# Kernel optimization log

Measured on AMD Instinct MI355X. Metric: run time of the kernel, lower is better.

## Reference

```python
import jax, jax.numpy as jnp
import numpy as np

B = 32768
INPUT_DIM = 2048
D = 2
HIDDEN = 128
V = 20          # output_dim (number of heads)
P = 6           # n_corr_params
R = 10          # r_lora = min(V // 2, 10)


def setup_inputs() -> dict:
    key = jax.random.key(0)
    ks = jax.random.split(key, 12)

    def lin(k, fan_in, shape):
        bound = 1.0 / np.sqrt(fan_in)
        return jax.random.uniform(k, shape, jnp.float32, -bound, bound)

    x = jax.random.normal(ks[0], (B, INPUT_DIM), jnp.float32)
    # encoder: Linear(input_dim, hidden) -> ReLU -> (Dropout=id) -> Linear(hidden, d)
    We1 = lin(ks[1], INPUT_DIM, (INPUT_DIM, HIDDEN))
    be1 = lin(ks[2], INPUT_DIM, (HIDDEN,))
    We2 = lin(ks[3], HIDDEN, (HIDDEN, D))
    be2 = lin(ks[4], HIDDEN, (D,))
    # 20 heads, each Linear(d, hidden) -> ReLU -> Linear(hidden, 6) -> Tanh,
    # stacked into batched weight tensors.
    W1 = lin(ks[5], D, (V, D, HIDDEN))
    b1 = lin(ks[6], D, (V, HIDDEN))
    W2 = lin(ks[7], HIDDEN, (V, HIDDEN, P))
    b2 = lin(ks[8], HIDDEN, (V, P))
    # LoRA params
    lora_A = jax.random.normal(ks[9], (D, R), jnp.float32) * 0.01
    lora_B = jax.random.normal(ks[10], (R, V * P), jnp.float32) * 0.01
    return {"x": x, "We1": We1, "be1": be1, "We2": We2, "be2": be2,
            "W1": W1, "b1": b1, "W2": W2, "b2": b2,
            "lora_A": lora_A, "lora_B": lora_B}


def reference(x, We1, be1, We2, be2, W1, b1, W2, b2, lora_A, lora_B):
    # encoder (nonlinear reduction; dropout is identity in eval)
    z = jax.nn.relu(x @ We1 + be1) @ We2 + be2            # [B, D]
    # all 20 heads as batched GEMMs
    h = jax.nn.relu(jnp.einsum('bd,vdh->bvh', z, W1) + b1)  # [B, V, HIDDEN]
    heads = jnp.tanh(jnp.einsum('bvh,vhp->bvp', h, W2) + b2)  # [B, V, P]
    # LoRA contribution, then outer tanh (note: double tanh, faithful to source)
    lora = (z @ lora_A @ lora_B).reshape(-1, V, P)         # [B, V, P]
    out = jnp.tanh(heads + 0.15 * lora)
    return (out, z)
```

## Files before the change

kernel.cpp:

```cpp
#include <hip/hip_runtime.h>
#include <hip/hip_bf16.h>
#include <cstdint>
#include <cstddef>

#define BDIM   32768
#define KDIM   2048
#define NDIM   128
#define VHEADS 20
#define PDIM   6
#define RLORA  10

#define BK      64
#define NCHUNK  (KDIM / BK)
#define OUT_ELEMS   (BDIM * VHEADS * PDIM)
#define WS_W_BYTES  (KDIM * NDIM * 2)

typedef __attribute__((ext_vector_type(8))) __bf16 bf16x8;
typedef __attribute__((ext_vector_type(4))) float f32x4;
typedef __attribute__((ext_vector_type(2))) float f32x2;
typedef __attribute__((ext_vector_type(4))) unsigned int u32x4;

union FragU { bf16x8 b; u32x4 u; };

__device__ __forceinline__ unsigned int cvt_pk_bf16(float lo, float hi) {
  unsigned int r;
  asm("v_cvt_pk_bf16_f32 %0, %1, %2" : "=v"(r) : "v"(lo), "v"(hi));
  return r;
}

__device__ __forceinline__ void gload_lds16(const void* g, void* l) {
  __builtin_amdgcn_global_load_lds(
      (const __attribute__((address_space(1))) void*)(g),
      (__attribute__((address_space(3))) void*)(l), 16, 0, 0);
}

__device__ __forceinline__ float fast_tanh(float x) {
  float ax = fabsf(x);
  float e  = __expf(-2.0f * ax);
  float t  = __fdividef(1.0f - e, 1.0f + e);
  return copysignf(t, x);
}

__global__ __launch_bounds__(256)
void k0_pack(const float* __restrict__ We1,
             const float* __restrict__ lA,
             const float* __restrict__ lB,
             unsigned short* __restrict__ wsw,
             float* __restrict__ wsM) {
  if (blockIdx.x == 128) {
    int t = threadIdx.x;
    if (t < 2 * VHEADS * PDIM) {
      int d  = t / (VHEADS * PDIM);
      int vp = t - d * (VHEADS * PDIM);
      float s = 0.f;
#pragma unroll
      for (int r = 0; r < RLORA; ++r)
        s = fmaf(lA[d * RLORA + r], lB[r * (VHEADS * PDIM) + vp], s);
      wsM[t] = s;
    }
    return;
  }
  int t    = blockIdx.x * 256 + threadIdx.x;
  int lane = t & 63;
  int blk  = t >> 6;
  int ks   = blk & 1;
  int nt   = (blk >> 1) & 7;
  int c    = blk >> 4;
  int n    = nt * 16 + (lane & 15);
  int kb   = c * 64 + ks * 32 + (lane >> 4) * 8;

  unsigned int u[4];
#pragma unroll
  for (int q = 0; q < 4; ++q) {
    float f0 = We1[(size_t)(kb + 2 * q + 0) * NDIM + n];
    float f1 = We1[(size_t)(kb + 2 * q + 1) * NDIM + n];
    __hip_bfloat16 h0 = __float2bfloat16(f0);
    __hip_bfloat16 h1 = __float2bfloat16(f1);
    u[q] = (unsigned int)*reinterpret_cast<unsigned short*>(&h0) |
           ((unsigned int)*reinterpret_cast<unsigned short*>(&h1) << 16);
  }
  *reinterpret_cast<u32x4*>(wsw + (size_t)t * 8) = u32x4{u[0], u[1], u[2], u[3]};
}

__global__ __launch_bounds__(512, 4)
void k1_fused(const float* __restrict__ x,
              const unsigned short* __restrict__ wp,
              const float* __restrict__ be1,
              const float* __restrict__ We2,
              const float* __restrict__ be2,
              const float* __restrict__ W1,
              const float* __restrict__ b1,
              const float* __restrict__ W2,
              const float* __restrict__ b2,
              const float* __restrict__ M,
              float* __restrict__ out,
              float* __restrict__ zout) {
  __shared__ char ldsA[2][16384] __attribute__((aligned(16)));
  __shared__ char ldsB[2][16384] __attribute__((aligned(16)));
  __shared__ float zpart2[64][2][2];
  __shared__ float zsh[64][2];

  const int tid  = threadIdx.x;
  const int lane = tid & 63;
  const int wv   = tid >> 6;
  const int wr   = wv & 3;
  const int wc   = wv >> 2;
  const int l15  = lane & 15;
  const int kgrp = lane >> 4;
  const int blk  = blockIdx.x;

  f32x4 acc[4];
#pragma unroll
  for (int i = 0; i < 4; ++i) acc[i] = f32x4{0.f, 0.f, 0.f, 0.f};

  auto STAGE = [&](int b, int c) {
#pragma unroll
    for (int q = 0; q < 2; ++q) {
      int s = tid + q * 512;
      int row = s >> 4;
      int g = (s & 15) ^ (row & 7);
      const float* asrc = x + (size_t)(blk * 64 + row) * KDIM + c * BK + g * 4;
      gload_lds16(asrc, &ldsA[b][s * 16]);
    }
#pragma unroll
    for (int q = 0; q < 2; ++q) {
      gload_lds16((const char*)wp + (size_t)c * 16384 + q * 8192 + tid * 16,
                  &ldsB[b][q * 8192 + tid * 16]);
    }
  };

  auto COMPUTE = [&](int b) {
    const int row = wr * 16 + l15;
    const char* abase = &ldsA[b][row * 256];
    const int rx = (row & 7) << 4;
    f32x4 A0 = *(const f32x4*)(abase + (((kgrp * 2 + 0) << 4) ^ rx));
    f32x4 A1 = *(const f32x4*)(abase + (((kgrp * 2 + 1) << 4) ^ rx));
    f32x4 A2 = *(const f32x4*)(abase + 128 + (((kgrp * 2 + 0) << 4) ^ rx));
    f32x4 A3 = *(const f32x4*)(abase + 128 + (((kgrp * 2 + 1) << 4) ^ rx));
    FragU a0, a1;
    a0.u = u32x4{cvt_pk_bf16(A0.x, A0.y), cvt_pk_bf16(A0.z, A0.w),
                 cvt_pk_bf16(A1.x, A1.y), cvt_pk_bf16(A1.z, A1.w)};
    a1.u = u32x4{cvt_pk_bf16(A2.x, A2.y), cvt_pk_bf16(A2.z, A2.w),
                 cvt_pk_bf16(A3.x, A3.y), cvt_pk_bf16(A3.z, A3.w)};
    const char* bbase = &ldsB[b][lane * 16];
#pragma unroll
    for (int nt = 0; nt < 4; ++nt) {
      FragU b0, b1;
      b0.u = *(const u32x4*)(bbase + ((wc * 4 + nt) * 2 + 0) * 1024);
      b1.u = *(const u32x4*)(bbase + ((wc * 4 + nt) * 2 + 1) * 1024);
      acc[nt] = __builtin_amdgcn_mfma_f32_16x16x32_bf16(a0.b, b0.b, acc[nt], 0, 0, 0);
      acc[nt] = __builtin_amdgcn_mfma_f32_16x16x32_bf16(a1.b, b1.b, acc[nt], 0, 0, 0);
    }
  };

  STAGE(0, 0);
  __syncthreads();

#pragma unroll 1
  for (int c = 0; c < NCHUNK; ++c) {
    int b = c & 1;
    if (c + 1 < NCHUNK) STAGE(b ^ 1, c + 1);
    COMPUTE(b);
    __syncthreads();
  }

  float part[4][2];
#pragma unroll
  for (int j = 0; j < 4; ++j) { part[j][0] = 0.f; part[j][1] = 0.f; }
#pragma unroll
  for (int nt = 0; nt < 4; ++nt) {
    int col = (wc * 4 + nt) * 16 + l15;
    float bb = be1[col];
    float w0 = We2[col * 2 + 0];
    float w1 = We2[col * 2 + 1];
#pragma unroll
    for (int j = 0; j < 4; ++j) {
      float h = acc[nt][j] + bb;
      h = h > 0.f ? h : 0.f;
      part[j][0] = fmaf(h, w0, part[j][0]);
      part[j][1] = fmaf(h, w1, part[j][1]);
    }
  }
#pragma unroll
  for (int m = 1; m < 16; m <<= 1) {
#pragma unroll
    for (int j = 0; j < 4; ++j) {
      part[j][0] += __shfl_xor(part[j][0], m, 64);
      part[j][1] += __shfl_xor(part[j][1], m, 64);
    }
  }
  if (l15 == 0) {
#pragma unroll
    for (int j = 0; j < 4; ++j) {
      int rl = wr * 16 + kgrp * 4 + j;
      zpart2[rl][wc][0] = part[j][0];
      zpart2[rl][wc][1] = part[j][1];
    }
  }
  __syncthreads();
  if (tid < 64) {
    float s0 = zpart2[tid][0][0] + zpart2[tid][1][0] + be2[0];
    float s1 = zpart2[tid][0][1] + zpart2[tid][1][1] + be2[1];
    zsh[tid][0] = s0;
    zsh[tid][1] = s1;
    f32x2 zz = {s0, s1};
    *(f32x2*)(zout + (size_t)(blk * 64 + tid) * 2) = zz;
  }
  __syncthreads();

  const int wvu = __builtin_amdgcn_readfirstlane(wv);
  float z0 = zsh[lane][0];
  float z1 = zsh[lane][1];
  float* orow = out + (size_t)(blk * 64 + lane) * (VHEADS * PDIM);

  auto head = [&](int v) {
    const float* w1a = W1 + (size_t)(v * 2 + 0) * NDIM;
    const float* w1b = W1 + (size_t)(v * 2 + 1) * NDIM;
    const float* bb1 = b1 + (size_t)v * NDIM;
    const float* w2  = W2 + (size_t)v * NDIM * PDIM;

    float p[6] = {0.f, 0.f, 0.f, 0.f, 0.f, 0.f};
#pragma unroll 4
    for (int h = 0; h < NDIM; ++h) {
      float hv = fmaf(z0, w1a[h], fmaf(z1, w1b[h], bb1[h]));
      hv = hv > 0.f ? hv : 0.f;
#pragma unroll
      for (int j = 0; j < 6; ++j) p[j] = fmaf(hv, w2[h * 6 + j], p[j]);
    }
    float o[6];
#pragma unroll
    for (int j = 0; j < 6; ++j) {
      float t1 = fast_tanh(p[j] + b2[v * PDIM + j]);
      float lo = fmaf(z0, M[v * PDIM + j], z1 * M[VHEADS * PDIM + v * PDIM + j]);
      o[j] = fast_tanh(fmaf(0.15f, lo, t1));
    }
    float* op = orow + v * PDIM;
    f32x2 o01 = {o[0], o[1]};
    f32x2 o23 = {o[2], o[3]};
    f32x2 o45 = {o[4], o[5]};
    __builtin_nontemporal_store(o01, (f32x2*)(op + 0));
    __builtin_nontemporal_store(o23, (f32x2*)(op + 2));
    __builtin_nontemporal_store(o45, (f32x2*)(op + 4));
  };

  head(wvu);
  head(wvu + 8);
  if (wvu < 4) head(wvu + 16);
}

extern "C" void kernel_launch(void* const* d_in, const int* in_sizes, int n_in,
                              void* d_out, int out_size, void* d_ws, size_t ws_size,
                              hipStream_t stream) {
  const float* x   = (const float*)d_in[0];
  const float* We1 = (const float*)d_in[1];
  const float* be1 = (const float*)d_in[2];
  const float* We2 = (const float*)d_in[3];
  const float* be2 = (const float*)d_in[4];
  const float* W1  = (const float*)d_in[5];
  const float* b1  = (const float*)d_in[6];
  const float* W2  = (const float*)d_in[7];
  const float* b2  = (const float*)d_in[8];
  const float* lA  = (const float*)d_in[9];
  const float* lB  = (const float*)d_in[10];

  float* out  = (float*)d_out;
  float* zout = out + OUT_ELEMS;
  unsigned short* wsw = (unsigned short*)d_ws;
  float* wsM = (float*)((char*)d_ws + WS_W_BYTES);

  hipLaunchKernelGGL(k0_pack, dim3(129), dim3(256), 0, stream,
                     We1, lA, lB, wsw, wsM);
  hipLaunchKernelGGL(k1_fused, dim3(BDIM / 64), dim3(512), 0, stream,
                     x, wsw, be1, We2, be2, W1, b1, W2, b2, wsM, out, zout);
}
```

Before: 102.7 us.

## Keep two K-chunks in flight with explicit vmcnt waits and split barriers

Restructures the main GEMM loop so two chunk loads are outstanding at once, using per-buffer LDS arrays, manual s_waitcnt vmcnt(4) waits and raw s_barrier with sched_barrier fences in place of __syncthreads. The aim is to hide global-to-LDS latency better by letting the next chunk's load overlap compute on the current one, rather than draining all loads each iteration. It relies on hand-counted outstanding loads (4 per stage), so correctness depends on exact instruction counts and on the compiler not inserting extra memory ops. There are now two barriers per chunk instead of one.

```diff
diff --git a/kernel.cpp b/kernel.cpp
--- a/kernel.cpp
+++ b/kernel.cpp
@@ -40,6 +40,8 @@
   float t  = __fdividef(1.0f - e, 1.0f + e);
   return copysignf(t, x);
 }
+
+#define SBAR() __builtin_amdgcn_sched_barrier(0)
 
 __global__ __launch_bounds__(256)
 void k0_pack(const float* __restrict__ We1,
@@ -95,8 +97,10 @@
               const float* __restrict__ M,
               float* __restrict__ out,
               float* __restrict__ zout) {
-  __shared__ char ldsA[2][16384] __attribute__((aligned(16)));
-  __shared__ char ldsB[2][16384] __attribute__((aligned(16)));
+  __shared__ char A0_[16384] __attribute__((aligned(16)));
+  __shared__ char A1_[16384] __attribute__((aligned(16)));
+  __shared__ char B0_[16384] __attribute__((aligned(16)));
+  __shared__ char B1_[16384] __attribute__((aligned(16)));
   __shared__ float zpart2[64][2][2];
   __shared__ float zsh[64][2];
 
@@ -113,25 +117,25 @@
 #pragma unroll
   for (int i = 0; i < 4; ++i) acc[i] = f32x4{0.f, 0.f, 0.f, 0.f};
 
-  auto STAGE = [&](int b, int c) {
+  auto STAGE = [&](char* Ad, char* Bd, int c) {
 #pragma unroll
     for (int q = 0; q < 2; ++q) {
       int s = tid + q * 512;
       int row = s >> 4;
       int g = (s & 15) ^ (row & 7);
       const float* asrc = x + (size_t)(blk * 64 + row) * KDIM + c * BK + g * 4;
-      gload_lds16(asrc, &ldsA[b][s * 16]);
+      gload_lds16(asrc, Ad + s * 16);
     }
 #pragma unroll
     for (int q = 0; q < 2; ++q) {
       gload_lds16((const char*)wp + (size_t)c * 16384 + q * 8192 + tid * 16,
-                  &ldsB[b][q * 8192 + tid * 16]);
+                  Bd + q * 8192 + tid * 16);
     }
   };
 
-  auto COMPUTE = [&](int b) {
+  auto COMPUTE = [&](const char* Ad, const char* Bd) {
     const int row = wr * 16 + l15;
-    const char* abase = &ldsA[b][row * 256];
+    const char* abase = Ad + row * 256;
     const int rx = (row & 7) << 4;
     f32x4 A0 = *(const f32x4*)(abase + (((kgrp * 2 + 0) << 4) ^ rx));
     f32x4 A1 = *(const f32x4*)(abase + (((kgrp * 2 + 1) << 4) ^ rx));
@@ -142,7 +146,7 @@
                  cvt_pk_bf16(A1.x, A1.y), cvt_pk_bf16(A1.z, A1.w)};
     a1.u = u32x4{cvt_pk_bf16(A2.x, A2.y), cvt_pk_bf16(A2.z, A2.w),
                  cvt_pk_bf16(A3.x, A3.y), cvt_pk_bf16(A3.z, A3.w)};
-    const char* bbase = &ldsB[b][lane * 16];
+    const char* bbase = Bd + lane * 16;
 #pragma unroll
     for (int nt = 0; nt < 4; ++nt) {
       FragU b0, b1;
@@ -153,16 +157,34 @@
     }
   };
 
-  STAGE(0, 0);
-  __syncthreads();
+  STAGE(A0_, B0_, 0);
+  STAGE(A1_, B1_, 1);
 
 #pragma unroll 1
-  for (int c = 0; c < NCHUNK; ++c) {
-    int b = c & 1;
-    if (c + 1 < NCHUNK) STAGE(b ^ 1, c + 1);
-    COMPUTE(b);
-    __syncthreads();
-  }
+  for (int cc = 0; cc < NCHUNK / 2 - 1; ++cc) {
+    asm volatile("s_waitcnt vmcnt(4)" ::: "memory");
+    SBAR();
+    __builtin_amdgcn_s_barrier();
+    COMPUTE(A0_, B0_);
+    __builtin_amdgcn_s_barrier();
+    SBAR();
+    STAGE(A0_, B0_, 2 * cc + 2);
+    asm volatile("s_waitcnt vmcnt(4)" ::: "memory");
+    SBAR();
+    __builtin_amdgcn_s_barrier();
+    COMPUTE(A1_, B1_);
+    __builtin_amdgcn_s_barrier();
+    SBAR();
+    STAGE(A1_, B1_, 2 * cc + 3);
+  }
+  asm volatile("s_waitcnt vmcnt(4)" ::: "memory");
+  SBAR();
+  __builtin_amdgcn_s_barrier();
+  COMPUTE(A0_, B0_);
+  asm volatile("s_waitcnt vmcnt(0)" ::: "memory");
+  SBAR();
+  __builtin_amdgcn_s_barrier();
+  COMPUTE(A1_, B1_);
 
   float part[4][2];
 #pragma unroll
```

After: 95.87 us (median of 2 runs). 1.07x faster.

## Halve row tile, load B fragments directly to registers, barrier-free per-wave pipeline

Applied to the files above, without the earlier changes.

The block tile shrinks from 64 to 32 rows with 256 threads and twice as many blocks. Each wave now stages only its own A rows into LDS. The packed We1 fragments are loaded straight into registers with inline global_load_dwordx4 instead of through LDS. The K loop is double-buffered with explicit vmcnt waits and sched barriers in place of __syncthreads, which removes block-wide synchronisation and LDS traffic for B. The cost is that each block re-reads all of We1 from cache, so B-operand global/L2 traffic doubles, and correctness now depends on hand-counted vmcnt values.

```diff
diff --git a/kernel.cpp b/kernel.cpp
--- a/kernel.cpp
+++ b/kernel.cpp
@@ -10,6 +10,7 @@
 #define PDIM   6
 #define RLORA  10
 
+#define BM      32
 #define BK      64
 #define NCHUNK  (KDIM / BK)
 #define OUT_ELEMS   (BDIM * VHEADS * PDIM)
@@ -40,6 +41,11 @@
   float t  = __fdividef(1.0f - e, 1.0f + e);
   return copysignf(t, x);
 }
+
+#define SBAR() __builtin_amdgcn_sched_barrier(0)
+#define GL16(dst, addr, OFFSTR) \
+  asm volatile("global_load_dwordx4 %0, %1, off offset:" OFFSTR \
+               : "=v"(dst) : "v"(addr))
 
 __global__ __launch_bounds__(256)
 void k0_pack(const float* __restrict__ We1,
@@ -82,7 +88,7 @@
   *reinterpret_cast<u32x4*>(wsw + (size_t)t * 8) = u32x4{u[0], u[1], u[2], u[3]};
 }
 
-__global__ __launch_bounds__(512, 4)
+__global__ __launch_bounds__(256, 4)
 void k1_fused(const float* __restrict__ x,
               const unsigned short* __restrict__ wp,
               const float* __restrict__ be1,
@@ -95,44 +101,52 @@
               const float* __restrict__ M,
               float* __restrict__ out,
               float* __restrict__ zout) {
-  __shared__ char ldsA[2][16384] __attribute__((aligned(16)));
-  __shared__ char ldsB[2][16384] __attribute__((aligned(16)));
-  __shared__ float zpart2[64][2][2];
-  __shared__ float zsh[64][2];
+  __shared__ char A0_[16384] __attribute__((aligned(16)));
+  __shared__ char A1_[16384] __attribute__((aligned(16)));
+  __shared__ float zpart2[32][2][2];
+  __shared__ float zsh[32][2];
 
   const int tid  = threadIdx.x;
   const int lane = tid & 63;
   const int wv   = tid >> 6;
-  const int wr   = wv & 3;
-  const int wc   = wv >> 2;
+  const int wr   = wv & 1;
+  const int wc   = wv >> 1;
   const int l15  = lane & 15;
   const int kgrp = lane >> 4;
   const int blk  = blockIdx.x;
 
+  const char* bwave = (const char*)wp + wc * 8192 + lane * 16 + 4096;
+
   f32x4 acc[4];
 #pragma unroll
   for (int i = 0; i < 4; ++i) acc[i] = f32x4{0.f, 0.f, 0.f, 0.f};
 
-  auto STAGE = [&](int b, int c) {
-#pragma unroll
-    for (int q = 0; q < 2; ++q) {
-      int s = tid + q * 512;
-      int row = s >> 4;
-      int g = (s & 15) ^ (row & 7);
-      const float* asrc = x + (size_t)(blk * 64 + row) * KDIM + c * BK + g * 4;
-      gload_lds16(asrc, &ldsA[b][s * 16]);
-    }
-#pragma unroll
-    for (int q = 0; q < 2; ++q) {
-      gload_lds16((const char*)wp + (size_t)c * 16384 + q * 8192 + tid * 16,
-                  &ldsB[b][q * 8192 + tid * 16]);
+  auto STAGE_A = [&](char* Ad, int c) {
+#pragma unroll
+    for (int q = 0; q < 4; ++q) {
+      int lr = q * 4 + (lane >> 4);
+      const float* asrc = x + (size_t)(blk * BM + wr * 16 + lr) * KDIM + c * BK
+                          + ((l15 ^ (lr & 7)) << 2);
+      gload_lds16(asrc, Ad + wv * 4096 + q * 1024);
     }
   };
 
-  auto COMPUTE = [&](int b) {
-    const int row = wr * 16 + l15;
-    const char* abase = &ldsA[b][row * 256];
-    const int rx = (row & 7) << 4;
+  FragU bf[8];
+  auto LOADB = [&](int c) {
+    const char* p = bwave + (size_t)c * 16384;
+    GL16(bf[0].u, p, "-4096");
+    GL16(bf[1].u, p, "-3072");
+    GL16(bf[2].u, p, "-2048");
+    GL16(bf[3].u, p, "-1024");
+    GL16(bf[4].u, p, "0");
+    GL16(bf[5].u, p, "1024");
+    GL16(bf[6].u, p, "2048");
+    GL16(bf[7].u, p, "3072");
+  };
+
+  auto COMPUTE = [&](const char* Ad) {
+    const char* abase = Ad + wv * 4096 + l15 * 256;
+    const int rx = (l15 & 7) << 4;
     f32x4 A0 = *(const f32x4*)(abase + (((kgrp * 2 + 0) << 4) ^ rx));
     f32x4 A1 = *(const f32x4*)(abase + (((kgrp * 2 + 1) << 4) ^ rx));
     f32x4 A2 = *(const f32x4*)(abase + 128 + (((kgrp * 2 + 0) << 4) ^ rx));
@@ -142,26 +156,36 @@
                  cvt_pk_bf16(A1.x, A1.y), cvt_pk_bf16(A1.z, A1.w)};
     a1.u = u32x4{cvt_pk_bf16(A2.x, A2.y), cvt_pk_bf16(A2.z, A2.w),
                  cvt_pk_bf16(A3.x, A3.y), cvt_pk_bf16(A3.z, A3.w)};
-    const char* bbase = &ldsB[b][lane * 16];
-#pragma unroll
-    for (int nt = 0; nt < 4; ++nt) {
-      FragU b0, b1;
-      b0.u = *(const u32x4*)(bbase + ((wc * 4 + nt) * 2 + 0) * 1024);
-      b1.u = *(const u32x4*)(bbase + ((wc * 4 + nt) * 2 + 1) * 1024);
-      acc[nt] = __builtin_amdgcn_mfma_f32_16x16x32_bf16(a0.b, b0.b, acc[nt], 0, 0, 0);
-      acc[nt] = __builtin_amdgcn_mfma_f32_16x16x32_bf16(a1.b, b1.b, acc[nt], 0, 0, 0);
-    }
+    acc[0] = __builtin_amdgcn_mfma_f32_16x16x32_bf16(a0.b, bf[0].b, acc[0], 0, 0, 0);
+    acc[0] = __builtin_amdgcn_mfma_f32_16x16x32_bf16(a1.b, bf[1].b, acc[0], 0, 0, 0);
+    acc[1] = __builtin_amdgcn_mfma_f32_16x16x32_bf16(a0.b, bf[2].b, acc[1], 0, 0, 0);
+    acc[1] = __builtin_amdgcn_mfma_f32_16x16x32_bf16(a1.b, bf[3].b, acc[1], 0, 0, 0);
+    acc[2] = __builtin_amdgcn_mfma_f32_16x16x32_bf16(a0.b, bf[4].b, acc[2], 0, 0, 0);
+    acc[2] = __builtin_amdgcn_mfma_f32_16x16x32_bf16(a1.b, bf[5].b, acc[2], 0, 0, 0);
+    acc[3] = __builtin_amdgcn_mfma_f32_16x16x32_bf16(a0.b, bf[6].b, acc[3], 0, 0, 0);
+    acc[3] = __builtin_amdgcn_mfma_f32_16x16x32_bf16(a1.b, bf[7].b, acc[3], 0, 0, 0);
   };
 
-  STAGE(0, 0);
-  __syncthreads();
+  STAGE_A(A0_, 0);
 
 #pragma unroll 1
-  for (int c = 0; c < NCHUNK; ++c) {
-    int b = c & 1;
-    if (c + 1 < NCHUNK) STAGE(b ^ 1, c + 1);
-    COMPUTE(b);
-    __syncthreads();
+  for (int cc = 0; cc < NCHUNK / 2; ++cc) {
+    LOADB(2 * cc);
+    STAGE_A(A1_, 2 * cc + 1);
+    asm volatile("s_waitcnt vmcnt(4)" ::: "memory");
+    SBAR();
+    COMPUTE(A0_);
+    SBAR();
+    LOADB(2 * cc + 1);
+    if (cc + 1 < NCHUNK / 2) STAGE_A(A0_, 2 * cc + 2);
+    if (cc + 1 < NCHUNK / 2) {
+      asm volatile("s_waitcnt vmcnt(4)" ::: "memory");
+    } else {
+      asm volatile("s_waitcnt vmcnt(0)" ::: "memory");
+    }
+    SBAR();
+    COMPUTE(A1_);
+    SBAR();
   }
 
   float part[4][2];
@@ -198,20 +222,21 @@
     }
   }
   __syncthreads();
-  if (tid < 64) {
+  if (tid < BM) {
     float s0 = zpart2[tid][0][0] + zpart2[tid][1][0] + be2[0];
     float s1 = zpart2[tid][0][1] + zpart2[tid][1][1] + be2[1];
     zsh[tid][0] = s0;
     zsh[tid][1] = s1;
     f32x2 zz = {s0, s1};
-    *(f32x2*)(zout + (size_t)(blk * 64 + tid) * 2) = zz;
+    *(f32x2*)(zout + (size_t)(blk * BM + tid) * 2) = zz;
   }
   __syncthreads();
 
-  const int wvu = __builtin_amdgcn_readfirstlane(wv);
-  float z0 = zsh[lane][0];
-  float z1 = zsh[lane][1];
-  float* orow = out + (size_t)(blk * 64 + lane) * (VHEADS * PDIM);
+  const int srow = tid & 31;
+  const int slot = tid >> 5;
+  float z0 = zsh[srow][0];
+  float z1 = zsh[srow][1];
+  float* orow = out + (size_t)(blk * BM + srow) * (VHEADS * PDIM);
 
   auto head = [&](int v) {
     const float* w1a = W1 + (size_t)(v * 2 + 0) * NDIM;
@@ -243,9 +268,9 @@
     __builtin_nontemporal_store(o45, (f32x2*)(op + 4));
   };
 
-  head(wvu);
-  head(wvu + 8);
-  if (wvu < 4) head(wvu + 16);
+  head(slot);
+  head(slot + 8);
+  if (slot < 4) head(slot + 16);
 }
 
 extern "C" void kernel_launch(void* const* d_in, const int* in_sizes, int n_in,
@@ -270,6 +295,6 @@
 
   hipLaunchKernelGGL(k0_pack, dim3(129), dim3(256), 0, stream,
                      We1, lA, lB, wsw, wsM);
-  hipLaunchKernelGGL(k1_fused, dim3(BDIM / 64), dim3(512), 0, stream,
+  hipLaunchKernelGGL(k1_fused, dim3(BDIM / BM), dim3(256), 0, stream,
                      x, wsw, be1, We2, be2, W1, b1, W2, b2, wsM, out, zout);
 }
```

After: 158.8 us. 54.6% more time.
